# Performance work log

Measured on AMD Instinct MI355X. Metric: run time of the kernel, lower is better.

Reference implementation:

```python
import jax, jax.numpy as jnp
import numpy as np

N = 100000   # nodes
E = 400000   # edges
G = 2000     # graphs in batch
F0 = 84      # num_features_xd
F2 = 840     # num_features_xd * 10


def setup_inputs() -> dict:
    key = jax.random.key(0)
    ks = jax.random.split(key, 8)
    x = jax.random.normal(ks[0], (N, F0), dtype=jnp.float32)
    edge_index = jax.random.randint(ks[1], (2, E), 0, N)
    batch = jnp.sort(jax.random.randint(ks[2], (N,), 0, G))

    def lin(k, fan_in, fan_out):
        bound = 1.0 / np.sqrt(fan_in)
        kw, kb = jax.random.split(k)
        W = jax.random.uniform(kw, (fan_in, fan_out), jnp.float32, -bound, bound)
        b = jax.random.uniform(kb, (fan_out,), jnp.float32, -bound, bound)
        return W, b

    W1, b1 = lin(ks[3], F0, F0)          # GINConv.nn of conv1
    W2, b2 = lin(ks[4], F0, F2)          # GINConv.nn of conv2
    Wf1, bf1 = lin(ks[5], 2 * F2, 1024)  # fc_g[0]
    Wf2, bf2 = lin(ks[6], 1024, 384)     # fc_g[3]
    return dict(x=x, edge_index=edge_index, batch=batch,
                W1=W1, b1=b1, W2=W2, b2=b2,
                Wf1=Wf1, bf1=bf1, Wf2=Wf2, bf2=bf2)


def _gin_conv(h, src, dst, W, b):
    # GINConv with default eps=0: nn((1+eps)*h + sum_{j in N(i)} h_j)
    agg = jax.ops.segment_sum(h[src], dst, num_segments=N)  # scatter-add over edges
    return (h + agg) @ W + b


def reference(x, edge_index, batch, W1, b1, W2, b2, Wf1, bf1, Wf2, bf2):
    src, dst = edge_index[0], edge_index[1]
    h1 = jax.nn.relu(_gin_conv(x, src, dst, W1, b1))    # [N, 84]
    h2 = jax.nn.relu(_gin_conv(h1, src, dst, W2, b2))   # [N, 840]
    # global_max_pool / global_add_pool over graphs
    pool_max = jax.ops.segment_max(h2, batch, num_segments=G)  # [G, 840]
    pool_sum = jax.ops.segment_sum(h2, batch, num_segments=G)  # [G, 840]
    xg = jnp.concatenate([pool_max, pool_sum], axis=1)          # [G, 1680]
    # fc_g: Linear->ReLU->(Dropout=id in eval)->Linear
    xg = jax.nn.relu(xg @ Wf1 + bf1) @ Wf2 + bf2                # [G, 384]
    return (xg, h2)
```

## Files before the change

### kernel.cpp

```cpp
#include <hip/hip_runtime.h>
#include <math.h>

#define NN 100000
#define NE 400000
#define NG 2000
#define F0 84
#define F2 840
#define FH 1024
#define FO 384
#define NT2 6250

typedef __attribute__((ext_vector_type(8))) short bf16x8;
typedef __attribute__((ext_vector_type(4))) float f32x4;

__device__ inline short f2bf(float f) {
    union { float f; unsigned u; } v; v.f = f;
    unsigned r = (v.u + 0x7FFFu + ((v.u >> 16) & 1u)) >> 16;
    return (short)r;
}
__device__ inline float b2f(short s) {
    union { unsigned u; float f; } v;
    v.u = ((unsigned)(unsigned short)s) << 16;
    return v.f;
}

#define S1 (8*3*64)
#define S2 (56*3*64)
#define S3 (64*53*64)
#define S4 (24*32*64)
#define PACK_TOT (S1 + S2 + S3 + S4)
#define NB_DEG  1563
#define NB_CAST 4688
#define NB_PACK 1088

__device__ inline void pack_one(const float* __restrict__ W, short* __restrict__ P,
                                int K, int N, int KB, int CT, int idx) {
    int lane = idx & 63;
    int t    = idx >> 6;
    int kb   = t % KB;
    int ct   = t / KB;
    int col  = ct * 16 + (lane & 15);
    int k0   = kb * 32 + ((lane >> 4) << 3);
    bf16x8 v;
#pragma unroll
    for (int j = 0; j < 8; ++j) {
        int k = k0 + j;
        float f = (k < K && col < N) ? W[(size_t)k * N + col] : 0.f;
        v[j] = f2bf(f);
    }
    *reinterpret_cast<bf16x8*>(P + (size_t)idx * 8) = v;
}

__global__ void front_kernel(const int* __restrict__ dst, int* __restrict__ deg,
                             const float* __restrict__ x, short* __restrict__ Xb,
                             const float* __restrict__ W1, short* __restrict__ P1,
                             const float* __restrict__ W2, short* __restrict__ P2,
                             const float* __restrict__ Wf1, short* __restrict__ P3,
                             const float* __restrict__ Wf2, short* __restrict__ P4) {
    int bid = blockIdx.x;
    if (bid < NB_DEG) {
        int e = bid * 256 + threadIdx.x;
        if (e < NE) atomicAdd(&deg[dst[e]], 1);
        return;
    }
    bid -= NB_DEG;
    if (bid < NB_CAST) {
        int idx = bid * 256 + threadIdx.x;
        if (idx < NN * 12) {
            int n = idx / 12;
            int c = idx - n * 12;
            int k0 = c * 8;
            bf16x8 v;
#pragma unroll
            for (int j = 0; j < 8; ++j) {
                int k = k0 + j;
                v[j] = (k < F0) ? f2bf(x[(size_t)n * F0 + k]) : (short)0;
            }
            *reinterpret_cast<bf16x8*>(Xb + (size_t)n * 96 + k0) = v;
        }
        return;
    }
    bid -= NB_CAST;
    int idx = bid * 256 + threadIdx.x;
    if (idx < S1) { pack_one(W1, P1, F0, F0, 3, 8, idx); return; }
    idx -= S1;
    if (idx < S2) { pack_one(W2, P2, F0, F2, 3, 56, idx); return; }
    idx -= S2;
    if (idx < S3) { pack_one(Wf1, P3, 1680, FH, 53, 64, idx); return; }
    idx -= S3;
    if (idx < S4) { pack_one(Wf2, P4, FH, FO, 32, 24, idx); return; }
}

__global__ void scan_ph1(const int* __restrict__ deg, int* __restrict__ rowptr,
                         int* __restrict__ bsum) {
    __shared__ int s[1024];
    int t = threadIdx.x;
    int i = blockIdx.x * 1024 + t;
    int v = (i < NN) ? deg[i] : 0;
    s[t] = v;
    __syncthreads();
    for (int d = 1; d < 1024; d <<= 1) {
        int u = (t >= d) ? s[t - d] : 0;
        __syncthreads();
        s[t] += u;
        __syncthreads();
    }
    if (i < NN) rowptr[i] = s[t] - v;
    if (t == 1023) bsum[blockIdx.x] = s[t];
}

__global__ void scan_ph23(int* __restrict__ rowptr, const int* __restrict__ bsum,
                          int* __restrict__ cnt, int nb) {
    __shared__ int s[128];
    int t = threadIdx.x;
    int b = blockIdx.x;
    if (t < 128) s[t] = (t < b && t < nb) ? bsum[t] : 0;
    __syncthreads();
    for (int d = 64; d >= 1; d >>= 1) {
        if (t < d) s[t] += s[t + d];
        __syncthreads();
    }
    int off = s[0];
    int i = b * 1024 + t;
    if (i < NN) {
        rowptr[i] += off;
        cnt[i] = 0;
    }
    if (i == 0) rowptr[NN] = NE;
}

__global__ void edge_fill(const int* __restrict__ src, const int* __restrict__ dst,
                          const int* __restrict__ rowptr, int* __restrict__ cnt,
                          int* __restrict__ eid) {
    int e = blockIdx.x * blockDim.x + threadIdx.x;
    if (e >= NE) return;
    int d = dst[e];
    int p = rowptr[d] + atomicAdd(&cnt[d], 1);
    eid[p] = src[e];
}

template <int CTW, int NWAVES, bool OUTBF16>
__global__ void conv_fused(const short* __restrict__ H,
                           const int* __restrict__ rowptr,
                           const int* __restrict__ eid,
                           const short* __restrict__ Bp,
                           const float* __restrict__ bias,
                           void* __restrict__ Cout,
                           int Nbias, int ldc, int ncols) {
    __shared__ short Alds[3 * 512];
    int rt = blockIdx.x;
    int t  = threadIdx.x;

    for (int item = t; item < 192; item += NWAVES * 64) {
        int r = item / 12;
        int c = item - r * 12;
        int n = rt * 16 + r;
        int off = c * 8;
        bf16x8 sv = *reinterpret_cast<const bf16x8*>(H + (size_t)n * 96 + off);
        float acc[8];
#pragma unroll
        for (int j = 0; j < 8; ++j) acc[j] = b2f(sv[j]);
        int e0 = rowptr[n], e1 = rowptr[n + 1];
        for (int e = e0; e < e1; ++e) {
            int s = eid[e];
            bf16x8 v = *reinterpret_cast<const bf16x8*>(H + (size_t)s * 96 + off);
#pragma unroll
            for (int j = 0; j < 8; ++j) acc[j] += b2f(v[j]);
        }
        bf16x8 o;
#pragma unroll
        for (int j = 0; j < 8; ++j) o[j] = f2bf(acc[j]);
        int kb = c >> 2, q = c & 3;
        *reinterpret_cast<bf16x8*>(&Alds[(kb * 512) + (q * 16 + r) * 8]) = o;
    }
    __syncthreads();

    int wave = t >> 6;
    int lane = t & 63;
    f32x4 acc[CTW];
#pragma unroll
    for (int u = 0; u < CTW; ++u) acc[u] = (f32x4){0.f, 0.f, 0.f, 0.f};
    const short* Bbase = Bp + (size_t)(wave * CTW) * 3 * 512 + lane * 8;
#pragma unroll
    for (int kb = 0; kb < 3; ++kb) {
        bf16x8 a = *reinterpret_cast<const bf16x8*>(&Alds[kb * 512 + lane * 8]);
#pragma unroll
        for (int u = 0; u < CTW; ++u) {
            bf16x8 b = *reinterpret_cast<const bf16x8*>(Bbase + ((size_t)u * 3 + kb) * 512);
            acc[u] = __builtin_amdgcn_mfma_f32_16x16x32_bf16(a, b, acc[u], 0, 0, 0);
        }
    }
    int row0 = rt * 16 + ((lane >> 4) << 2);
#pragma unroll
    for (int u = 0; u < CTW; ++u) {
        int col = (wave * CTW + u) * 16 + (lane & 15);
        float bi = (col < Nbias) ? bias[col] : 0.f;
        if (col < ncols) {
#pragma unroll
            for (int r = 0; r < 4; ++r) {
                float v = fmaxf(acc[u][r] + bi, 0.f);
                if (OUTBF16) ((short*)Cout)[(size_t)(row0 + r) * ldc + col] = f2bf(v);
                else         ((float*)Cout)[(size_t)(row0 + r) * ldc + col] = v;
            }
        }
    }
}

__global__ __launch_bounds__(512) void conv2_part(
        const short* __restrict__ H, const int* __restrict__ rowptr,
        const int* __restrict__ eid, const short* __restrict__ Bp,
        const float* __restrict__ bias, float* __restrict__ h2,
        float* __restrict__ Pmax, float* __restrict__ Psum) {
    __shared__ short Alds[3 * 512];
    int rt = blockIdx.x;
    int t  = threadIdx.x;

    if (t < 192) {
        int r = t / 12;
        int c = t - r * 12;
        int n = rt * 16 + r;
        int off = c * 8;
        bf16x8 sv = *reinterpret_cast<const bf16x8*>(H + (size_t)n * 96 + off);
        float acc[8];
#pragma unroll
        for (int j = 0; j < 8; ++j) acc[j] = b2f(sv[j]);
        int e0 = rowptr[n], e1 = rowptr[n + 1];
        for (int e = e0; e < e1; ++e) {
            int s = eid[e];
            bf16x8 v = *reinterpret_cast<const bf16x8*>(H + (size_t)s * 96 + off);
#pragma unroll
            for (int j = 0; j < 8; ++j) acc[j] += b2f(v[j]);
        }
        bf16x8 o;
#pragma unroll
        for (int j = 0; j < 8; ++j) o[j] = f2bf(acc[j]);
        int kb = c >> 2, q = c & 3;
        *reinterpret_cast<bf16x8*>(&Alds[(kb * 512) + (q * 16 + r) * 8]) = o;
    }
    __syncthreads();

    int wave = t >> 6;
    int lane = t & 63;
    f32x4 acc[7];
#pragma unroll
    for (int u = 0; u < 7; ++u) acc[u] = (f32x4){0.f, 0.f, 0.f, 0.f};
    const short* Bbase = Bp + (size_t)(wave * 7) * 3 * 512 + lane * 8;
#pragma unroll
    for (int kb = 0; kb < 3; ++kb) {
        bf16x8 a = *reinterpret_cast<const bf16x8*>(&Alds[kb * 512 + lane * 8]);
#pragma unroll
        for (int u = 0; u < 7; ++u) {
            bf16x8 b = *reinterpret_cast<const bf16x8*>(Bbase + ((size_t)u * 3 + kb) * 512);
            acc[u] = __builtin_amdgcn_mfma_f32_16x16x32_bf16(a, b, acc[u], 0, 0, 0);
        }
    }
    int row0 = rt * 16 + ((lane >> 4) << 2);
#pragma unroll
    for (int u = 0; u < 7; ++u) {
        int col = (wave * 7 + u) * 16 + (lane & 15);
        if (col < F2) {
            float bi = bias[col];
            float m = -INFINITY, sm = 0.f;
#pragma unroll
            for (int r = 0; r < 4; ++r) {
                float v = fmaxf(acc[u][r] + bi, 0.f);
                h2[(size_t)(row0 + r) * F2 + col] = v;
                m = fmaxf(m, v);
                sm += v;
            }
            m = fmaxf(m, __shfl_xor(m, 16));
            m = fmaxf(m, __shfl_xor(m, 32));
            sm += __shfl_xor(sm, 16);
            sm += __shfl_xor(sm, 32);
            if (lane < 16) {
                Pmax[(size_t)rt * F2 + col] = m;
                Psum[(size_t)rt * F2 + col] = sm;
            }
        }
    }
}

__global__ void pool_kernel(const float* __restrict__ h2,
                            const int* __restrict__ batch,
                            const float* __restrict__ Pmax,
                            const float* __restrict__ Psum,
                            short* __restrict__ A3) {
    int g = blockIdx.x;
    int t = threadIdx.x;
    __shared__ int se[2];
    if (t < 2) {
        int target = g + t;
        int lo = 0, hi = NN;
        while (lo < hi) {
            int mid = (lo + hi) >> 1;
            if (batch[mid] < target) lo = mid + 1; else hi = mid;
        }
        se[t] = lo;
    }
    __syncthreads();
    int s = se[0], e = se[1];
    int t0 = (s + 15) >> 4;
    int t1 = e >> 4;
    if (t < 210) {
        int c4 = t * 4;
        float sm0 = 0.f, sm1 = 0.f, sm2 = 0.f, sm3 = 0.f;
        float mx0 = -INFINITY, mx1 = -INFINITY, mx2 = -INFINITY, mx3 = -INFINITY;
        if (t1 >= t0) {
            for (int tile = t0; tile < t1; ++tile) {
                float4 pm = *reinterpret_cast<const float4*>(Pmax + (size_t)tile * F2 + c4);
                float4 ps = *reinterpret_cast<const float4*>(Psum + (size_t)tile * F2 + c4);
                mx0 = fmaxf(mx0, pm.x); mx1 = fmaxf(mx1, pm.y);
                mx2 = fmaxf(mx2, pm.z); mx3 = fmaxf(mx3, pm.w);
                sm0 += ps.x; sm1 += ps.y; sm2 += ps.z; sm3 += ps.w;
            }
            for (int n = s; n < (t0 << 4); ++n) {
                float4 v = *reinterpret_cast<const float4*>(h2 + (size_t)n * F2 + c4);
                sm0 += v.x; sm1 += v.y; sm2 += v.z; sm3 += v.w;
                mx0 = fmaxf(mx0, v.x); mx1 = fmaxf(mx1, v.y);
                mx2 = fmaxf(mx2, v.z); mx3 = fmaxf(mx3, v.w);
            }
            for (int n = (t1 << 4); n < e; ++n) {
                float4 v = *reinterpret_cast<const float4*>(h2 + (size_t)n * F2 + c4);
                sm0 += v.x; sm1 += v.y; sm2 += v.z; sm3 += v.w;
                mx0 = fmaxf(mx0, v.x); mx1 = fmaxf(mx1, v.y);
                mx2 = fmaxf(mx2, v.z); mx3 = fmaxf(mx3, v.w);
            }
        } else {
            for (int n = s; n < e; ++n) {
                float4 v = *reinterpret_cast<const float4*>(h2 + (size_t)n * F2 + c4);
                sm0 += v.x; sm1 += v.y; sm2 += v.z; sm3 += v.w;
                mx0 = fmaxf(mx0, v.x); mx1 = fmaxf(mx1, v.y);
                mx2 = fmaxf(mx2, v.z); mx3 = fmaxf(mx3, v.w);
            }
        }
        short* xr = A3 + (size_t)g * 1696;
        short4 mo, so;
        mo.x = f2bf(mx0); mo.y = f2bf(mx1); mo.z = f2bf(mx2); mo.w = f2bf(mx3);
        so.x = f2bf(sm0); so.y = f2bf(sm1); so.z = f2bf(sm2); so.w = f2bf(sm3);
        *reinterpret_cast<short4*>(xr + c4)      = mo;
        *reinterpret_cast<short4*>(xr + F2 + c4) = so;
    }
    if (t >= 210 && t < 214) {
        short4 z = {0, 0, 0, 0};
        *reinterpret_cast<short4*>(A3 + (size_t)g * 1696 + 1680 + (t - 210) * 4) = z;
    }
}

template <int CTW, bool RELU, bool OUTBF16>
__global__ void gemmN(const short* __restrict__ A, const short* __restrict__ Bp,
                      const float* __restrict__ bias, void* __restrict__ Cout,
                      int Kp, int Nbias, int ldc, int ncols,
                      int rowTiles, int ctGroups) {
    int gid = blockIdx.x * blockDim.x + threadIdx.x;
    int w   = gid >> 6;
    if (w >= rowTiles * ctGroups) return;
    int lane = gid & 63;
    int rt = w / ctGroups;
    int cg = w - rt * ctGroups;
    int KB = Kp >> 5;
    const short* Ap = A + (size_t)(rt * 16 + (lane & 15)) * Kp + ((lane >> 4) << 3);
    const short* Bbase = Bp + (size_t)(cg * CTW) * KB * 512 + lane * 8;
    f32x4 acc[CTW];
#pragma unroll
    for (int u = 0; u < CTW; ++u) acc[u] = (f32x4){0.f, 0.f, 0.f, 0.f};
    for (int kb = 0; kb < KB; ++kb) {
        bf16x8 a = *reinterpret_cast<const bf16x8*>(Ap + kb * 32);
#pragma unroll
        for (int u = 0; u < CTW; ++u) {
            bf16x8 b = *reinterpret_cast<const bf16x8*>(Bbase + ((size_t)u * KB + kb) * 512);
            acc[u] = __builtin_amdgcn_mfma_f32_16x16x32_bf16(a, b, acc[u], 0, 0, 0);
        }
    }
    int row0 = rt * 16 + ((lane >> 4) << 2);
#pragma unroll
    for (int u = 0; u < CTW; ++u) {
        int col = (cg * CTW + u) * 16 + (lane & 15);
        float bi = (col < Nbias) ? bias[col] : 0.f;
        if (col < ncols) {
#pragma unroll
            for (int r = 0; r < 4; ++r) {
                int row = row0 + r;
                float v = acc[u][r] + bi;
                if (RELU) v = fmaxf(v, 0.f);
                if (OUTBF16) ((short*)Cout)[(size_t)row * ldc + col] = f2bf(v);
                else         ((float*)Cout)[(size_t)row * ldc + col] = v;
            }
        }
    }
}

extern "C" void kernel_launch(void* const* d_in, const int* in_sizes, int n_in,
                              void* d_out, int out_size, void* d_ws, size_t ws_size,
                              hipStream_t stream) {
    const float* x    = (const float*)d_in[0];
    const int*   ei   = (const int*)d_in[1];
    const int*   batch= (const int*)d_in[2];
    const float* W1   = (const float*)d_in[3];
    const float* b1   = (const float*)d_in[4];
    const float* W2   = (const float*)d_in[5];
    const float* b2   = (const float*)d_in[6];
    const float* Wf1  = (const float*)d_in[7];
    const float* bf1  = (const float*)d_in[8];
    const float* Wf2  = (const float*)d_in[9];
    const float* bf2  = (const float*)d_in[10];

    const int* src = ei;
    const int* dst = ei + NE;

    float* xg_out = (float*)d_out;
    float* h2     = (float*)d_out + (size_t)NG * FO;

    short* Xb   = (short*)d_ws;
    short* h1   = Xb + (size_t)NN * 96;
    short* A3   = h1 + (size_t)NN * 96;
    short* fc1o = A3 + (size_t)NG * 1696;
    short* W1p  = fc1o + (size_t)NG * FH;
    short* W2p  = W1p + (size_t)S1 * 8;
    short* Wf1p = W2p + (size_t)S2 * 8;
    short* Wf2p = Wf1p + (size_t)S3 * 8;
    int*   deg  = (int*)(Wf2p + (size_t)S4 * 8);
    int*   cnt  = deg + NN;
    int*   rowptr = cnt + NN;
    int*   bsum = rowptr + NN + 1;
    int*   eid  = bsum + 128;
    float* Pmax = (float*)(eid + NE);
    float* Psum = Pmax + (size_t)NT2 * F2;

    const int blk = 256;
    auto cdiv = [](long long a, long long b) { return (int)((a + b - 1) / b); };
    const int nb1024 = cdiv(NN, 1024);

    hipMemsetAsync(deg, 0, (size_t)NN * sizeof(int), stream);
    front_kernel<<<NB_DEG + NB_CAST + NB_PACK, blk, 0, stream>>>(
        dst, deg, x, Xb, W1, W1p, W2, W2p, Wf1, Wf1p, Wf2, Wf2p);

    scan_ph1<<<nb1024, 1024, 0, stream>>>(deg, rowptr, bsum);
    scan_ph23<<<nb1024, 1024, 0, stream>>>(rowptr, bsum, cnt, nb1024);
    edge_fill<<<cdiv(NE, blk), blk, 0, stream>>>(src, dst, rowptr, cnt, eid);

    conv_fused<2, 4, true><<<NT2, 256, 0, stream>>>(
        Xb, rowptr, eid, W1p, b1, h1, F0, 96, 96);

    conv2_part<<<NT2, 512, 0, stream>>>(h1, rowptr, eid, W2p, b2, h2, Pmax, Psum);

    pool_kernel<<<NG, blk, 0, stream>>>(h2, batch, Pmax, Psum, A3);

    gemmN<2, true, true><<<cdiv(125LL * 32 * 64, blk), blk, 0, stream>>>(
        A3, Wf1p, bf1, fc1o, 1696, FH, FH, FH, 125, 32);
    gemmN<2, false, false><<<cdiv(125LL * 12 * 64, blk), blk, 0, stream>>>(
        fc1o, Wf2p, bf2, xg_out, 1024, FO, FO, FO, 125, 12);
}
```

Before: 355.1 us.

## Split gather into 4-wide items, widen conv1 block, fuse edge fill with cast/pack

The neighbor-sum gather now uses 384 threads per 16-row tile, each handling 4 bf16 features instead of 8, so twice as many threads hide the latency of the irregular loads. Conv1 moves to 512-thread blocks with one column tile per wave. The degree count becomes its own small kernel, and the CSR edge fill is merged into the launch that casts x and packs the weights, removing one separate launch. In exchange, each thread issues smaller loads and repeats the rowptr and eid reads, and the degree atomics now run without the cast/pack work alongside them.

```diff
diff --git a/kernel.cpp b/kernel.cpp
--- a/kernel.cpp
+++ b/kernel.cpp
@@ -11,6 +11,7 @@
 #define NT2 6250
 
 typedef __attribute__((ext_vector_type(8))) short bf16x8;
+typedef __attribute__((ext_vector_type(4))) short bf16x4;
 typedef __attribute__((ext_vector_type(4))) float f32x4;
 
 __device__ inline short f2bf(float f) {
@@ -29,7 +30,7 @@
 #define S3 (64*53*64)
 #define S4 (24*32*64)
 #define PACK_TOT (S1 + S2 + S3 + S4)
-#define NB_DEG  1563
+#define NB_FILL 1563
 #define NB_CAST 4688
 #define NB_PACK 1088
 
@@ -51,44 +52,9 @@
     *reinterpret_cast<bf16x8*>(P + (size_t)idx * 8) = v;
 }
 
-__global__ void front_kernel(const int* __restrict__ dst, int* __restrict__ deg,
-                             const float* __restrict__ x, short* __restrict__ Xb,
-                             const float* __restrict__ W1, short* __restrict__ P1,
-                             const float* __restrict__ W2, short* __restrict__ P2,
-                             const float* __restrict__ Wf1, short* __restrict__ P3,
-                             const float* __restrict__ Wf2, short* __restrict__ P4) {
-    int bid = blockIdx.x;
-    if (bid < NB_DEG) {
-        int e = bid * 256 + threadIdx.x;
-        if (e < NE) atomicAdd(&deg[dst[e]], 1);
-        return;
-    }
-    bid -= NB_DEG;
-    if (bid < NB_CAST) {
-        int idx = bid * 256 + threadIdx.x;
-        if (idx < NN * 12) {
-            int n = idx / 12;
-            int c = idx - n * 12;
-            int k0 = c * 8;
-            bf16x8 v;
-#pragma unroll
-            for (int j = 0; j < 8; ++j) {
-                int k = k0 + j;
-                v[j] = (k < F0) ? f2bf(x[(size_t)n * F0 + k]) : (short)0;
-            }
-            *reinterpret_cast<bf16x8*>(Xb + (size_t)n * 96 + k0) = v;
-        }
-        return;
-    }
-    bid -= NB_CAST;
-    int idx = bid * 256 + threadIdx.x;
-    if (idx < S1) { pack_one(W1, P1, F0, F0, 3, 8, idx); return; }
-    idx -= S1;
-    if (idx < S2) { pack_one(W2, P2, F0, F2, 3, 56, idx); return; }
-    idx -= S2;
-    if (idx < S3) { pack_one(Wf1, P3, 1680, FH, 53, 64, idx); return; }
-    idx -= S3;
-    if (idx < S4) { pack_one(Wf2, P4, FH, FO, 32, 24, idx); return; }
+__global__ void edge_deg(const int* __restrict__ dst, int* __restrict__ deg) {
+    int e = blockIdx.x * blockDim.x + threadIdx.x;
+    if (e < NE) atomicAdd(&deg[dst[e]], 1);
 }
 
 __global__ void scan_ph1(const int* __restrict__ deg, int* __restrict__ rowptr,
@@ -129,49 +95,91 @@
     if (i == 0) rowptr[NN] = NE;
 }
 
-__global__ void edge_fill(const int* __restrict__ src, const int* __restrict__ dst,
-                          const int* __restrict__ rowptr, int* __restrict__ cnt,
-                          int* __restrict__ eid) {
-    int e = blockIdx.x * blockDim.x + threadIdx.x;
-    if (e >= NE) return;
-    int d = dst[e];
-    int p = rowptr[d] + atomicAdd(&cnt[d], 1);
-    eid[p] = src[e];
-}
-
-template <int CTW, int NWAVES, bool OUTBF16>
-__global__ void conv_fused(const short* __restrict__ H,
-                           const int* __restrict__ rowptr,
-                           const int* __restrict__ eid,
-                           const short* __restrict__ Bp,
-                           const float* __restrict__ bias,
-                           void* __restrict__ Cout,
-                           int Nbias, int ldc, int ncols) {
+__global__ void fill_cast_pack(const int* __restrict__ src, const int* __restrict__ dst,
+                               const int* __restrict__ rowptr, int* __restrict__ cnt,
+                               int* __restrict__ eid,
+                               const float* __restrict__ x, short* __restrict__ Xb,
+                               const float* __restrict__ W1, short* __restrict__ P1,
+                               const float* __restrict__ W2, short* __restrict__ P2,
+                               const float* __restrict__ Wf1, short* __restrict__ P3,
+                               const float* __restrict__ Wf2, short* __restrict__ P4) {
+    int bid = blockIdx.x;
+    if (bid < NB_FILL) {
+        int e = bid * 256 + threadIdx.x;
+        if (e < NE) {
+            int d = dst[e];
+            int p = rowptr[d] + atomicAdd(&cnt[d], 1);
+            eid[p] = src[e];
+        }
+        return;
+    }
+    bid -= NB_FILL;
+    if (bid < NB_CAST) {
+        int idx = bid * 256 + threadIdx.x;
+        if (idx < NN * 12) {
+            int n = idx / 12;
+            int c = idx - n * 12;
+            int k0 = c * 8;
+            bf16x8 v;
+#pragma unroll
+            for (int j = 0; j < 8; ++j) {
+                int k = k0 + j;
+                v[j] = (k < F0) ? f2bf(x[(size_t)n * F0 + k]) : (short)0;
+            }
+            *reinterpret_cast<bf16x8*>(Xb + (size_t)n * 96 + k0) = v;
+        }
+        return;
+    }
+    bid -= NB_CAST;
+    int idx = bid * 256 + threadIdx.x;
+    if (idx < S1) { pack_one(W1, P1, F0, F0, 3, 8, idx); return; }
+    idx -= S1;
+    if (idx < S2) { pack_one(W2, P2, F0, F2, 3, 56, idx); return; }
+    idx -= S2;
+    if (idx < S3) { pack_one(Wf1, P3, 1680, FH, 53, 64, idx); return; }
+    idx -= S3;
+    if (idx < S4) { pack_one(Wf2, P4, FH, FO, 32, 24, idx); return; }
+}
+
+__device__ inline void gather_item4(const short* __restrict__ H,
+                                    const int* __restrict__ rowptr,
+                                    const int* __restrict__ eid,
+                                    int n, int r, int c4, short* __restrict__ ldsTile) {
+    int k0 = c4 * 4;
+    bf16x4 sv = *reinterpret_cast<const bf16x4*>(H + (size_t)n * 96 + k0);
+    float acc[4];
+#pragma unroll
+    for (int j = 0; j < 4; ++j) acc[j] = b2f(sv[j]);
+    int e0 = rowptr[n], e1 = rowptr[n + 1];
+    for (int e = e0; e < e1; ++e) {
+        int s = eid[e];
+        bf16x4 v = *reinterpret_cast<const bf16x4*>(H + (size_t)s * 96 + k0);
+#pragma unroll
+        for (int j = 0; j < 4; ++j) acc[j] += b2f(v[j]);
+    }
+    bf16x4 o;
+#pragma unroll
+    for (int j = 0; j < 4; ++j) o[j] = f2bf(acc[j]);
+    int kb = k0 >> 5;
+    int q  = (k0 >> 3) & 3;
+    int h  = k0 & 7;
+    *reinterpret_cast<bf16x4*>(&ldsTile[kb * 512 + (q * 16 + r) * 8 + h]) = o;
+}
+
+template <int CTW, bool OUTBF16>
+__global__ __launch_bounds__(512) void conv_fused(
+        const short* __restrict__ H, const int* __restrict__ rowptr,
+        const int* __restrict__ eid, const short* __restrict__ Bp,
+        const float* __restrict__ bias, void* __restrict__ Cout,
+        int Nbias, int ldc, int ncols) {
     __shared__ short Alds[3 * 512];
     int rt = blockIdx.x;
     int t  = threadIdx.x;
 
-    for (int item = t; item < 192; item += NWAVES * 64) {
-        int r = item / 12;
-        int c = item - r * 12;
-        int n = rt * 16 + r;
-        int off = c * 8;
-        bf16x8 sv = *reinterpret_cast<const bf16x8*>(H + (size_t)n * 96 + off);
-        float acc[8];
-#pragma unroll
-        for (int j = 0; j < 8; ++j) acc[j] = b2f(sv[j]);
-        int e0 = rowptr[n], e1 = rowptr[n + 1];
-        for (int e = e0; e < e1; ++e) {
-            int s = eid[e];
-            bf16x8 v = *reinterpret_cast<const bf16x8*>(H + (size_t)s * 96 + off);
-#pragma unroll
-            for (int j = 0; j < 8; ++j) acc[j] += b2f(v[j]);
-        }
-        bf16x8 o;
-#pragma unroll
-        for (int j = 0; j < 8; ++j) o[j] = f2bf(acc[j]);
-        int kb = c >> 2, q = c & 3;
-        *reinterpret_cast<bf16x8*>(&Alds[(kb * 512) + (q * 16 + r) * 8]) = o;
+    if (t < 384) {
+        int r  = t / 24;
+        int c4 = t - r * 24;
+        gather_item4(H, rowptr, eid, rt * 16 + r, r, c4, Alds);
     }
     __syncthreads();
 
@@ -215,27 +223,10 @@
     int rt = blockIdx.x;
     int t  = threadIdx.x;
 
-    if (t < 192) {
-        int r = t / 12;
-        int c = t - r * 12;
-        int n = rt * 16 + r;
-        int off = c * 8;
-        bf16x8 sv = *reinterpret_cast<const bf16x8*>(H + (size_t)n * 96 + off);
-        float acc[8];
-#pragma unroll
-        for (int j = 0; j < 8; ++j) acc[j] = b2f(sv[j]);
-        int e0 = rowptr[n], e1 = rowptr[n + 1];
-        for (int e = e0; e < e1; ++e) {
-            int s = eid[e];
-            bf16x8 v = *reinterpret_cast<const bf16x8*>(H + (size_t)s * 96 + off);
-#pragma unroll
-            for (int j = 0; j < 8; ++j) acc[j] += b2f(v[j]);
-        }
-        bf16x8 o;
-#pragma unroll
-        for (int j = 0; j < 8; ++j) o[j] = f2bf(acc[j]);
-        int kb = c >> 2, q = c & 3;
-        *reinterpret_cast<bf16x8*>(&Alds[(kb * 512) + (q * 16 + r) * 8]) = o;
+    if (t < 384) {
+        int r  = t / 24;
+        int c4 = t - r * 24;
+        gather_item4(H, rowptr, eid, rt * 16 + r, r, c4, Alds);
     }
     __syncthreads();
 
@@ -431,14 +422,15 @@
     const int nb1024 = cdiv(NN, 1024);
 
     hipMemsetAsync(deg, 0, (size_t)NN * sizeof(int), stream);
-    front_kernel<<<NB_DEG + NB_CAST + NB_PACK, blk, 0, stream>>>(
-        dst, deg, x, Xb, W1, W1p, W2, W2p, Wf1, Wf1p, Wf2, Wf2p);
-
+    edge_deg<<<NB_FILL, blk, 0, stream>>>(dst, deg);
     scan_ph1<<<nb1024, 1024, 0, stream>>>(deg, rowptr, bsum);
     scan_ph23<<<nb1024, 1024, 0, stream>>>(rowptr, bsum, cnt, nb1024);
-    edge_fill<<<cdiv(NE, blk), blk, 0, stream>>>(src, dst, rowptr, cnt, eid);
-
-    conv_fused<2, 4, true><<<NT2, 256, 0, stream>>>(
+
+    fill_cast_pack<<<NB_FILL + NB_CAST + NB_PACK, blk, 0, stream>>>(
+        src, dst, rowptr, cnt, eid,
+        x, Xb, W1, W1p, W2, W2p, Wf1, Wf1p, Wf2, Wf2p);
+
+    conv_fused<1, true><<<NT2, 512, 0, stream>>>(
         Xb, rowptr, eid, W1p, b1, h1, F0, 96, 96);
 
     conv2_part<<<NT2, 512, 0, stream>>>(h1, rowptr, eid, W2p, b2, h2, Pmax, Psum);
```

Measured after the change: 368.6 us. +3.8%, slower.
